# Optimization experiments

Measured on AMD Instinct MI355X. Metric: run time of the kernel, lower is better.

## Reference

```python
import jax, jax.numpy as jnp
import numpy as np
from jax import lax

# ---- module constants (match init_kwargs) ----
B, C, H, W = 8, 32, 128, 128
OUT = 32
RB = 1                      # refer_band
GB = (1, 1)                 # init_guard_band
GB_MAX = 3
PAD = GB[0] + RB            # replication pad on all 4 sides (=2)
KH = GB[0] + GB[1] + 2 * RB # kernel_size[0] = 4
KW = 4                      # kernel_size[1]
N = KH * KW                 # 16 ring sampling points
EPS = 1e-5


def _gen_prf():
    """Ring offsets (top,right,bottom,left blocks), matches _gen_prf_grid."""
    rb, gb = RB, GB
    h_prf = (rb + gb[0]) * 2 + 1
    w_prf = (rb + gb[1]) * 2 + 1
    xs = np.arange(-(rb + gb[0]), rb + gb[0] + 1)
    ys = np.arange(-(rb + gb[1]), rb + gb[1] + 1)
    X, Y = np.meshgrid(xs, ys, indexing='ij')
    def ring(A):
        t = A[0:rb, 0:w_prf - rb]
        r = A[0:h_prf - rb, w_prf - rb:w_prf]
        d = A[h_prf - rb:h_prf, rb:w_prf]
        l = A[rb:h_prf, 0:rb]
        return np.concatenate([t.ravel(), r.ravel(), d.ravel(), l.ravel()])
    return ring(X).astype(np.float32), ring(Y).astype(np.float32)

PRF_X, PRF_Y = _gen_prf()  # each (N,)


def _conv(x, w, b, pad, stride=(1, 1)):
    out = lax.conv_general_dilated(
        x, w, stride, [(pad[0], pad[0]), (pad[1], pad[1])],
        dimension_numbers=('NCHW', 'OIHW', 'NCHW'))
    return out + b[None, :, None, None]


def _bn(x, gamma, beta):
    # training-mode batchnorm (biased variance), matching torch default
    m = jnp.mean(x, (0, 2, 3), keepdims=True)
    v = jnp.var(x, (0, 2, 3), keepdims=True)
    return (x - m) * jax.lax.rsqrt(v + EPS) * gamma[None, :, None, None] + beta[None, :, None, None]


def _sample(x_flat, ix, iy, Wp, h, w):
    # x_flat: (B, C, Hp*Wp); ix, iy: (B, h, w, N) int -> (B, C, h, w, N)
    b = ix.shape[0]
    c = x_flat.shape[1]
    idx = (ix * Wp + iy).reshape(b, 1, -1)
    g = jnp.take_along_axis(x_flat, idx, axis=2)
    return g.reshape(b, c, h, w, N)


def _forward(x, w_vrt, b_vrt, g_vrt, be_vrt, w_hrz, b_hrz, g_hrz, be_hrz, w_pk, b_pk):
    b, c, h, w = x.shape
    x_pad = jnp.pad(x, ((0, 0), (0, 0), (PAD, PAD), (PAD, PAD)), mode='edge')
    Hp, Wp = x_pad.shape[2], x_pad.shape[3]
    x_flat = x_pad.reshape(b, c, Hp * Wp)

    # ---- BandEst: per-pixel guard-band widths in 4 directions (B,4,H,W) ----
    v = jax.nn.sigmoid(_bn(_conv(x, w_vrt, b_vrt, (GB_MAX, 0)), g_vrt, be_vrt)) * (GB_MAX - 1)
    hz = jax.nn.sigmoid(_bn(_conv(x, w_hrz, b_hrz, (0, GB_MAX)), g_hrz, be_hrz)) * (GB_MAX - 1)
    gb = jnp.concatenate([v, hz], axis=1)

    # ---- reference-cell sampling positions p = center + ring + learned move ----
    base_x = (jnp.arange(h, dtype=x.dtype) + PAD)[None, :, None, None]
    base_y = (jnp.arange(w, dtype=x.dtype) + PAD)[None, None, :, None]
    p_x = base_x + jnp.asarray(PRF_X)[None, None, None, :]  # (1,H,1,N)->bcast
    p_y = base_y + jnp.asarray(PRF_Y)[None, None, None, :]

    n4 = N // 4  # points per ring side (t,r,d,l ordering)
    def rep(g2):  # (B,H,W) -> (B,H,W,n4)
        return jnp.broadcast_to(g2[..., None], (b, h, w, n4))
    zeros = jnp.zeros((b, h, w, n4), x.dtype)
    move_x = jnp.concatenate([-rep(gb[:, 0]), zeros, rep(gb[:, 1]), zeros], -1)
    move_y = jnp.concatenate([zeros, rep(gb[:, 3]), zeros, -rep(gb[:, 2])], -1)
    p_x = p_x + move_x  # (B,H,W,N)
    p_y = p_y + move_y

    # ---- bilinear (two-corner) gather, mirrors torch q_lt/q_rb/g_lt/g_rb ----
    q_lt_x = jnp.floor(lax.stop_gradient(p_x))
    q_lt_y = jnp.floor(lax.stop_gradient(p_y))
    q_rb_x, q_rb_y = q_lt_x + 1, q_lt_y + 1
    q_lt_xi = jnp.clip(q_lt_x, 0, Hp - 1).astype(jnp.int32)
    q_lt_yi = jnp.clip(q_lt_y, 0, Wp - 1).astype(jnp.int32)
    q_rb_xi = jnp.clip(q_rb_x, 0, Hp - 1).astype(jnp.int32)
    q_rb_yi = jnp.clip(q_rb_y, 0, Wp - 1).astype(jnp.int32)
    p_x = jnp.clip(p_x, 0, Hp - 1)
    p_y = jnp.clip(p_y, 0, Wp - 1)

    g_lt = (1 + (q_lt_xi.astype(p_x.dtype) - p_x)) * (1 + (q_lt_yi.astype(p_y.dtype) - p_y))
    g_rb = (1 - (q_rb_xi.astype(p_x.dtype) - p_x)) * (1 - (q_rb_yi.astype(p_y.dtype) - p_y))

    x_q_lt = _sample(x_flat, q_lt_xi, q_lt_yi, Wp, h, w)  # (B,C,H,W,N)
    x_q_rb = _sample(x_flat, q_rb_xi, q_rb_yi, Wp, h, w)
    x_r = g_lt[:, None] * x_q_lt + g_rb[:, None] * x_q_rb

    # center value x_c equals x itself (center indices land in the interior)
    x_prf = x[:, :, :, :, None] - x_r  # (B,C,H,W,N)

    # ---- _reshape_x_prf: (B,C,H,W,N) -> (B,C,H*KH,W*KW) ----
    xk = x_prf.reshape(b, c, h, w, KH, KW).transpose(0, 1, 2, 4, 3, 5).reshape(b, c, h * KH, w * KW)

    # ---- peak conv: kernel = stride = (KH,KW), no padding ----
    return _conv(xk, w_pk, b_pk, (0, 0), stride=(KH, KW))


def setup_inputs() -> dict:
    key = jax.random.key(0)
    ks = jax.random.split(key, 8)
    s = 0.05
    return {
        'x': jax.random.normal(ks[0], (B, C, H, W), jnp.float32),
        'w_vrt': jax.random.normal(ks[1], (2, C, 2 * GB_MAX + 1, 1), jnp.float32) * s,
        'b_vrt': jax.random.normal(ks[2], (2,), jnp.float32) * s,
        'g_vrt': jnp.ones((2,), jnp.float32),
        'be_vrt': jnp.zeros((2,), jnp.float32),
        'w_hrz': jax.random.normal(ks[3], (2, C, 1, 2 * GB_MAX + 1), jnp.float32) * s,
        'b_hrz': jax.random.normal(ks[4], (2,), jnp.float32) * s,
        'g_hrz': jnp.ones((2,), jnp.float32),
        'be_hrz': jnp.zeros((2,), jnp.float32),
        'w_pk': jax.random.normal(ks[5], (OUT, C, KH, KW), jnp.float32) * s,
        'b_pk': jax.random.normal(ks[6], (OUT,), jnp.float32) * s,
    }


def reference(x, w_vrt, b_vrt, g_vrt, be_vrt, w_hrz, b_hrz, g_hrz, be_hrz, w_pk, b_pk):
    return _forward(x, w_vrt, b_vrt, g_vrt, be_vrt, w_hrz, b_hrz, g_hrz, be_hrz, w_pk, b_pk)
```

## Files before the change

### kernel.cpp

```cpp
#include <hip/hip_runtime.h>
#include <math.h>

#define BB 8
#define CCH 32
#define HH 128
#define WW 128
#define OUTC 32
#define NPIX (BB*HH*WW)
#define HWP 131
#define NCONVBLK 2048

#define WS_XTB   0
#define WS_CONV4 (BB*HH*WW*CCH/2)
#define WS_PART  (WS_CONV4 + BB*HH*WW*4)
#define WS_WKB   (WS_PART + NCONVBLK*8)

#define TILE_USH (12*40*5*8)

typedef __attribute__((ext_vector_type(8))) short short8;
typedef __attribute__((ext_vector_type(4))) float f32x4;

__device__ __forceinline__ unsigned short f2bf(float f) {
    unsigned u = __float_as_uint(f);
    unsigned r = (u + 0x7FFFu + ((u >> 16) & 1u)) >> 16;
    return (unsigned short)r;
}
__device__ __forceinline__ unsigned cvtpk(float lo, float hi) {
    unsigned r;
    asm("v_cvt_pk_bf16_f32 %0, %1, %2" : "=v"(r) : "v"(lo), "v"(hi));
    return r;
}
__device__ __forceinline__ float bflo(unsigned w) { return __uint_as_float(w << 16); }
__device__ __forceinline__ float bfhi(unsigned w) { return __uint_as_float(w & 0xFFFF0000u); }

__global__ __launch_bounds__(256) void k_fused1(const float* __restrict__ x,
        const float* __restrict__ w_vrt, const float* __restrict__ b_vrt,
        const float* __restrict__ w_hrz, const float* __restrict__ b_hrz,
        const float* __restrict__ w_pk, float* __restrict__ ws) {
    __shared__ float red[4][64][4];
    __shared__ unsigned xrowp[16][65];
    int blk = blockIdx.x, t = threadIdx.x;
    if (blk < NCONVBLK) {
        int cb = blk;
        int idx0 = cb * 64;
        int b = idx0 >> 14, ij0 = idx0 & 16383, i = ij0 >> 7, j0c = ij0 & 127;
        int px = t & 63;
        int grp = __builtin_amdgcn_readfirstlane(t >> 6);
        float v0 = 0.f, v1 = 0.f, h0 = 0.f, h1 = 0.f;
        float cen_prev = 0.f;
        for (int c8 = 0; c8 < 8; c8++) {
            int c = grp * 8 + c8;
            const float* basec = x + ((size_t)(b*CCH + c))*HH*WW;
            #pragma unroll
            for (int k = 0; k < 7; k++) {
                float wv0 = w_vrt[c*7 + k], wv1 = w_vrt[224 + c*7 + k];
                int gr = i + k - 3;
                if (gr >= 0 && gr < HH) {
                    float xv = basec[(size_t)gr*WW + j0c + px];
                    v0 += wv0 * xv; v1 += wv1 * xv;
                    if (k == 3) {
                        if ((c8 & 1) == 0) cen_prev = xv;
                        else xrowp[grp*4 + (c8 >> 1)][px] = cvtpk(cen_prev, xv);
                    }
                }
                float wh0 = w_hrz[c*7 + k], wh1 = w_hrz[224 + c*7 + k];
                int gc = j0c + px + k - 3;
                if (gc >= 0 && gc < WW) {
                    float xh = basec[(size_t)i*WW + gc];
                    h0 += wh0 * xh; h1 += wh1 * xh;
                }
            }
        }
        red[grp][px][0] = v0; red[grp][px][1] = v1;
        red[grp][px][2] = h0; red[grp][px][3] = h1;
        __syncthreads();
        {
            unsigned* xtb4 = (unsigned*)(ws + WS_XTB);
            int bi = b*HH + i;
            #pragma unroll
            for (int u = 0; u < 4; u++) {
                int e = u*256 + t;
                int ppx = e >> 4, cp = e & 15;
                xtb4[((size_t)bi*WW + j0c + ppx)*16 + cp] = xrowp[cp][ppx];
            }
        }
        if (grp == 0) {
            float fv0 = red[0][px][0]+red[1][px][0]+red[2][px][0]+red[3][px][0] + b_vrt[0];
            float fv1 = red[0][px][1]+red[1][px][1]+red[2][px][1]+red[3][px][1] + b_vrt[1];
            float fh0 = red[0][px][2]+red[1][px][2]+red[2][px][2]+red[3][px][2] + b_hrz[0];
            float fh1 = red[0][px][3]+red[1][px][3]+red[2][px][3]+red[3][px][3] + b_hrz[1];
            float4* conv4 = (float4*)(ws + WS_CONV4);
            conv4[idx0 + px] = make_float4(fv0, fv1, fh0, fh1);
            float stv[8] = {fv0, fv1, fh0, fh1, fv0*fv0, fv1*fv1, fh0*fh0, fh1*fh1};
            #pragma unroll
            for (int u = 0; u < 8; u++) {
                float s = stv[u];
                for (int off = 32; off; off >>= 1) s += __shfl_down(s, off);
                if (px == 0) ws[WS_PART + cb*8 + u] = s;
            }
        }
    } else {
        unsigned short* wkb = (unsigned short*)(ws + WS_WKB);
        int e = (blk - NCONVBLK) * 2048 + t;
        for (int u = 0; u < 8; u++, e += 256) {
            int o = e >> 9, n = (e >> 5) & 15, c = e & 31;
            wkb[o*512 + n*32 + c] = f2bf(w_pk[((o*32 + c) << 4) + n]);
        }
    }
}

__device__ __forceinline__ short8 sample_frag(const unsigned short* tile,
        const float* xc8, const float* gbv, float fi, float fj, int n,
        float prx, float pry, int i0, int j0, int quad) {
    float mx = 0.f, my = 0.f;
    if (n < 4)       mx = -gbv[0];
    else if (n < 8)  my =  gbv[3];
    else if (n < 12) mx =  gbv[1];
    else             my = -gbv[2];
    float px = fi + prx + mx;
    float py = fj + pry + my;
    float qlx = floorf(px), qly = floorf(py);
    int qlxi = min(max((int)qlx, 0), HWP);
    int qlyi = min(max((int)qly, 0), HWP);
    int qrxi = min(max((int)qlx + 1, 0), HWP);
    int qryi = min(max((int)qly + 1, 0), HWP);
    float pxc = fminf(fmaxf(px, 0.f), (float)HWP);
    float pyc = fminf(fmaxf(py, 0.f), (float)HWP);
    float glt = (1.f + ((float)qlxi - pxc)) * (1.f + ((float)qlyi - pyc));
    float grb = (1.f - ((float)qrxi - pxc)) * (1.f - ((float)qryi - pyc));
    float nglt = -glt, ngrb = -grb;
    int ltr = min(max(qlxi - 2, 0), HH - 1), ltc = min(max(qlyi - 2, 0), WW - 1);
    int rbr = min(max(qrxi - 2, 0), HH - 1), rbc = min(max(qryi - 2, 0), WW - 1);
    int lt_off = (ltr - i0 + 4)*1600 + (ltc - j0 + 4)*40 + quad*8;
    int rb_off = (rbr - i0 + 4)*1600 + (rbc - j0 + 4)*40 + quad*8;
    uint4 lw = *(const uint4*)(tile + lt_off);
    uint4 rw = *(const uint4*)(tile + rb_off);
    float d0 = fmaf(nglt, bflo(lw.x), fmaf(ngrb, bflo(rw.x), xc8[0]));
    float d1 = fmaf(nglt, bfhi(lw.x), fmaf(ngrb, bfhi(rw.x), xc8[1]));
    float d2 = fmaf(nglt, bflo(lw.y), fmaf(ngrb, bflo(rw.y), xc8[2]));
    float d3 = fmaf(nglt, bfhi(lw.y), fmaf(ngrb, bfhi(rw.y), xc8[3]));
    float d4 = fmaf(nglt, bflo(lw.z), fmaf(ngrb, bflo(rw.z), xc8[4]));
    float d5 = fmaf(nglt, bfhi(lw.z), fmaf(ngrb, bfhi(rw.z), xc8[5]));
    float d6 = fmaf(nglt, bflo(lw.w), fmaf(ngrb, bflo(rw.w), xc8[6]));
    float d7 = fmaf(nglt, bfhi(lw.w), fmaf(ngrb, bfhi(rw.w), xc8[7]));
    uint4 bw;
    bw.x = cvtpk(d0, d1); bw.y = cvtpk(d2, d3);
    bw.z = cvtpk(d4, d5); bw.w = cvtpk(d6, d7);
    return *(short8*)&bw;
}

__device__ __forceinline__ void frac_setup(float pm, float& ng, int& m) {
    float qf = floorf(pm);
    int qi = min(max((int)qf, 0), HWP);
    float pmc = fminf(fmaxf(pm, 0.f), (float)HWP);
    ng = pmc - (float)qi - 1.f;
    m = min(max(qi - 2, 0), HH - 1);
}
__device__ __forceinline__ short8 samp1(const unsigned short* tile,
        const float* xc8, float ng, int off) {
    uint4 lw = *(const uint4*)(tile + off);
    float d0 = fmaf(ng, bflo(lw.x), xc8[0]);
    float d1 = fmaf(ng, bfhi(lw.x), xc8[1]);
    float d2 = fmaf(ng, bflo(lw.y), xc8[2]);
    float d3 = fmaf(ng, bfhi(lw.y), xc8[3]);
    float d4 = fmaf(ng, bflo(lw.z), xc8[4]);
    float d5 = fmaf(ng, bfhi(lw.z), xc8[5]);
    float d6 = fmaf(ng, bflo(lw.w), xc8[6]);
    float d7 = fmaf(ng, bfhi(lw.w), xc8[7]);
    uint4 bw;
    bw.x = cvtpk(d0, d1); bw.y = cvtpk(d2, d3);
    bw.z = cvtpk(d4, d5); bw.w = cvtpk(d6, d7);
    return *(short8*)&bw;
}

__global__ __launch_bounds__(256, 4) void k_main(const float* __restrict__ ws,
        const float* __restrict__ x,
        const float* __restrict__ g_vrt, const float* __restrict__ be_vrt,
        const float* __restrict__ g_hrz, const float* __restrict__ be_hrz,
        const float* __restrict__ b_pk, float* __restrict__ out) {
    __shared__ unsigned short tile[TILE_USH];
    __shared__ float racc[32][8];
    __shared__ float bnab_s[8];
    const unsigned short* xtb = (const unsigned short*)(ws + WS_XTB);
    const unsigned short* wkb = (const unsigned short*)(ws + WS_WKB);
    const float* part = ws + WS_PART;
    const float prfx[16] = {-2,-2,-2,-2, -2,-1, 0, 1,  2, 2, 2, 2, -1, 0, 1, 2};
    const float prfy[16] = {-2,-1, 0, 1,  2, 2, 2, 2, -1, 0, 1, 2, -2,-2,-2,-2};
    const int ioffs[16]  = {-2,-1, 0, 1, -2,-1, 0, 1, -1, 0, 1, 2, -1, 0, 1, 2};

    int t = threadIdx.x;
    int blk = ((blockIdx.x & 7) << 7) | (blockIdx.x >> 3);
    int b = blk >> 7;
    int i0 = ((blk >> 2) & 31) * 4;
    int j0 = (blk & 3) * 32;

    for (int s = t; s < 12*40*4; s += 256) {
        int q = s & 3, cc = (s >> 2) % 40, r = (s >> 2) / 40;
        int gr = min(max(i0 - 4 + r, 0), HH - 1);
        int gc = min(max(j0 - 4 + cc, 0), WW - 1);
        uint4 v = *(const uint4*)(xtb + (((size_t)(b*HH + gr))*WW + gc)*CCH + q*8);
        *(uint4*)(tile + ((r*40 + cc)*5 + q)*8) = v;
    }
    {
        int s8 = t & 7, chunk = t >> 3;
        float sum = 0.f;
        #pragma unroll 8
        for (int m = 0; m < 64; m++)
            sum += part[(size_t)(chunk*64 + m)*8 + s8];
        racc[chunk][s8] = sum;
    }
    __syncthreads();
    if (t < 8) {
        float tot = 0.f;
        #pragma unroll
        for (int c = 0; c < 32; c++) tot += racc[c][t];
        racc[0][t] = tot;
    }
    __syncthreads();
    if (t < 4) {
        const float cnt = (float)NPIX;
        float mean = racc[0][t] / cnt;
        float var  = racc[0][4 + t] / cnt - mean * mean;
        float gamma = (t < 2) ? g_vrt[t] : g_hrz[t - 2];
        float beta  = (t < 2) ? be_vrt[t] : be_hrz[t - 2];
        float a = gamma * rsqrtf(var + 1e-5f);
        bnab_s[t]     = a;
        bnab_s[4 + t] = beta - mean * a;
    }
    __syncthreads();

    int w = t >> 6, pl = t & 15, quad = (t >> 4) & 3;
    int ir = i0 + w;
    int pjA = j0 + pl, pjB = j0 + 16 + pl;
    int pixA = (b << 14) + ir * WW + pjA;
    int pixB = pixA + 16;
    int q8 = quad * 8;

    float xcA[8], xcB[8];
    {
        const float* xb = x + (size_t)b * CCH * HH * WW + (size_t)ir * WW;
        #pragma unroll
        for (int k = 0; k < 8; k++) {
            const float* p = xb + (size_t)(q8 + k) * (HH * WW);
            xcA[k] = p[pjA];
            xcB[k] = p[pjB];
        }
    }
    const float4* conv4 = (const float4*)(ws + WS_CONV4);
    float4 cvA = conv4[pixA], cvB = conv4[pixB];
    float gbvA[4], gbvB[4];
    gbvA[0] = 2.f / (1.f + expf(-(cvA.x * bnab_s[0] + bnab_s[4])));
    gbvA[1] = 2.f / (1.f + expf(-(cvA.y * bnab_s[1] + bnab_s[5])));
    gbvA[2] = 2.f / (1.f + expf(-(cvA.z * bnab_s[2] + bnab_s[6])));
    gbvA[3] = 2.f / (1.f + expf(-(cvA.w * bnab_s[3] + bnab_s[7])));
    gbvB[0] = 2.f / (1.f + expf(-(cvB.x * bnab_s[0] + bnab_s[4])));
    gbvB[1] = 2.f / (1.f + expf(-(cvB.y * bnab_s[1] + bnab_s[5])));
    gbvB[2] = 2.f / (1.f + expf(-(cvB.z * bnab_s[2] + bnab_s[6])));
    gbvB[3] = 2.f / (1.f + expf(-(cvB.w * bnab_s[3] + bnab_s[7])));

    f32x4 accA0 = {0.f,0.f,0.f,0.f}, accA1 = {0.f,0.f,0.f,0.f};
    f32x4 accB0 = {0.f,0.f,0.f,0.f}, accB1 = {0.f,0.f,0.f,0.f};
    float fi = (float)ir + 2.f;
    float fjA = (float)pjA + 2.f, fjB = (float)pjB + 2.f;

    short8 a0 = *(const short8*)(wkb + (size_t)pl * 512 + q8);
    short8 a1 = *(const short8*)(wkb + (size_t)(pl + 16) * 512 + q8);

    float ngA_ = 0.f, ngB_ = 0.f;
    int baseA_ = 0, baseB_ = 0;

    #pragma unroll
    for (int n = 0; n < 16; n++) {
        short8 na0 = a0, na1 = a1;
        if (n < 15) {
            na0 = *(const short8*)(wkb + (size_t)pl * 512 + (n+1)*32 + q8);
            na1 = *(const short8*)(wkb + (size_t)(pl + 16) * 512 + (n+1)*32 + q8);
        }
        if ((n & 3) == 0) {
            int g = n >> 2;
            float pmA, pmB;
            if (g == 0)      { pmA = (fi  - 2.f) - gbvA[0]; pmB = (fi  - 2.f) - gbvB[0]; }
            else if (g == 1) { pmA = (fjA + 2.f) + gbvA[3]; pmB = (fjB + 2.f) + gbvB[3]; }
            else if (g == 2) { pmA = (fi  + 2.f) + gbvA[1]; pmB = (fi  + 2.f) + gbvB[1]; }
            else             { pmA = (fjA - 2.f) - gbvA[2]; pmB = (fjB - 2.f) - gbvB[2]; }
            int mA, mB;
            frac_setup(pmA, ngA_, mA);
            frac_setup(pmB, ngB_, mB);
            if ((g & 1) == 0) {
                baseA_ = (mA - i0 + 4)*1600 + q8;
                baseB_ = (mB - i0 + 4)*1600 + q8;
            } else {
                baseA_ = (mA - j0 + 4)*40 + q8;
                baseB_ = (mB - j0 + 4)*40 + q8;
            }
        }
        short8 bfA, bfB;
        if (n == 11 || n == 15) {
            bfA = sample_frag(tile, xcA, gbvA, fi, fjA, n, prfx[n], prfy[n], i0, j0, quad);
            bfB = sample_frag(tile, xcB, gbvB, fi, fjB, n, prfx[n], prfy[n], i0, j0, quad);
        } else {
            int io = ioffs[n];
            int offA, offB;
            if (((n >> 2) & 1) == 0) {
                int cA = min(max(pjA + io, 0), WW - 1);
                int cB = min(max(pjB + io, 0), WW - 1);
                offA = baseA_ + (cA - j0 + 4)*40;
                offB = baseB_ + (cB - j0 + 4)*40;
            } else {
                int r  = min(max(ir + io, 0), HH - 1);
                int rt = (r - i0 + 4)*1600;
                offA = baseA_ + rt;
                offB = baseB_ + rt;
            }
            bfA = samp1(tile, xcA, ngA_, offA);
            bfB = samp1(tile, xcB, ngB_, offB);
        }
        accA0 = __builtin_amdgcn_mfma_f32_16x16x32_bf16(a0, bfA, accA0, 0, 0, 0);
        accA1 = __builtin_amdgcn_mfma_f32_16x16x32_bf16(a1, bfA, accA1, 0, 0, 0);
        accB0 = __builtin_amdgcn_mfma_f32_16x16x32_bf16(a0, bfB, accB0, 0, 0, 0);
        accB1 = __builtin_amdgcn_mfma_f32_16x16x32_bf16(a1, bfB, accB1, 0, 0, 0);
        a0 = na0; a1 = na1;
    }
    float* opA = out + (size_t)b * (OUTC*HH*WW) + ir * WW + pjA;
    float* opB = opA + 16;
    #pragma unroll
    for (int r = 0; r < 4; r++) {
        int o = quad*4 + r;
        float bo = b_pk[o], bo16 = b_pk[o + 16];
        opA[(size_t)o * (HH*WW)]        = accA0[r] + bo;
        opA[(size_t)(o + 16) * (HH*WW)] = accA1[r] + bo16;
        opB[(size_t)o * (HH*WW)]        = accB0[r] + bo;
        opB[(size_t)(o + 16) * (HH*WW)] = accB1[r] + bo16;
    }
}

extern "C" void kernel_launch(void* const* d_in, const int* in_sizes, int n_in,
                              void* d_out, int out_size, void* d_ws, size_t ws_size,
                              hipStream_t stream) {
    const float* x      = (const float*)d_in[0];
    const float* w_vrt  = (const float*)d_in[1];
    const float* b_vrt  = (const float*)d_in[2];
    const float* g_vrt  = (const float*)d_in[3];
    const float* be_vrt = (const float*)d_in[4];
    const float* w_hrz  = (const float*)d_in[5];
    const float* b_hrz  = (const float*)d_in[6];
    const float* g_hrz  = (const float*)d_in[7];
    const float* be_hrz = (const float*)d_in[8];
    const float* w_pk   = (const float*)d_in[9];
    const float* b_pk   = (const float*)d_in[10];
    float* ws  = (float*)d_ws;
    float* out = (float*)d_out;

    k_fused1<<<NCONVBLK + 8, 256, 0, stream>>>(x, w_vrt, b_vrt, w_hrz, b_hrz, w_pk, ws);
    k_main<<<1024, 256, 0, stream>>>(ws, x, g_vrt, be_vrt, g_hrz, be_hrz, b_pk, out);
}
```

Baseline: 147.1 us.

## Split band-estimation convs into row-strip vertical and row-wise horizontal blocks

Restructures the first kernel into separate block types. Vertical-conv blocks each cover 8 rows and keep 14 input rows in registers, so every loaded value is reused across rows. Horizontal-conv blocks each handle a full row with float2 loads, two pixels per thread. This cuts the redundant 7x global reads per pixel from the old fused per-pixel loop, at the cost of more registers per thread and a changed workspace layout for conv outputs and partial BN statistics.

```diff
diff --git a/kernel.cpp b/kernel.cpp
--- a/kernel.cpp
+++ b/kernel.cpp
@@ -8,12 +8,13 @@
 #define OUTC 32
 #define NPIX (BB*HH*WW)
 #define HWP 131
-#define NCONVBLK 2048
 
 #define WS_XTB   0
-#define WS_CONV4 (BB*HH*WW*CCH/2)
-#define WS_PART  (WS_CONV4 + BB*HH*WW*4)
-#define WS_WKB   (WS_PART + NCONVBLK*8)
+#define WS_VO2   2097152
+#define WS_HO2   (WS_VO2 + NPIX*2)
+#define WS_PARTV (WS_HO2 + NPIX*2)
+#define WS_PARTH (WS_PARTV + 2048*4)
+#define WS_WKB   (WS_PARTH + 1024*4)
 
 #define TILE_USH (12*40*5*8)
 
@@ -37,71 +38,146 @@
         const float* __restrict__ w_vrt, const float* __restrict__ b_vrt,
         const float* __restrict__ w_hrz, const float* __restrict__ b_hrz,
         const float* __restrict__ w_pk, float* __restrict__ ws) {
-    __shared__ float red[4][64][4];
-    __shared__ unsigned xrowp[16][65];
+    __shared__ unsigned sbuf[12288];
     int blk = blockIdx.x, t = threadIdx.x;
-    if (blk < NCONVBLK) {
-        int cb = blk;
-        int idx0 = cb * 64;
-        int b = idx0 >> 14, ij0 = idx0 & 16383, i = ij0 >> 7, j0c = ij0 & 127;
+    if (blk < 256) {
+        int jh = blk & 1, istr = (blk >> 1) & 15, b = blk >> 5;
+        int i0 = istr * 8;
         int px = t & 63;
-        int grp = __builtin_amdgcn_readfirstlane(t >> 6);
-        float v0 = 0.f, v1 = 0.f, h0 = 0.f, h1 = 0.f;
-        float cen_prev = 0.f;
+        int sub = __builtin_amdgcn_readfirstlane(t >> 6);
+        int col = jh * 64 + px;
+        unsigned* xp = sbuf;
+        float* red_v = (float*)(sbuf + 8192);
+        float vo[8][2];
+        #pragma unroll
+        for (int r = 0; r < 8; r++) { vo[r][0] = 0.f; vo[r][1] = 0.f; }
+        float prev[8];
         for (int c8 = 0; c8 < 8; c8++) {
-            int c = grp * 8 + c8;
+            int c = sub * 8 + c8;
             const float* basec = x + ((size_t)(b*CCH + c))*HH*WW;
-            #pragma unroll
-            for (int k = 0; k < 7; k++) {
-                float wv0 = w_vrt[c*7 + k], wv1 = w_vrt[224 + c*7 + k];
-                int gr = i + k - 3;
-                if (gr >= 0 && gr < HH) {
-                    float xv = basec[(size_t)gr*WW + j0c + px];
-                    v0 += wv0 * xv; v1 += wv1 * xv;
-                    if (k == 3) {
-                        if ((c8 & 1) == 0) cen_prev = xv;
-                        else xrowp[grp*4 + (c8 >> 1)][px] = cvtpk(cen_prev, xv);
-                    }
+            float xv[14];
+            #pragma unroll
+            for (int rr = 0; rr < 14; rr++) {
+                int gr = i0 - 3 + rr;
+                xv[rr] = ((unsigned)gr < (unsigned)HH) ? basec[(size_t)gr*WW + col] : 0.f;
+            }
+            #pragma unroll
+            for (int r = 0; r < 8; r++) {
+                #pragma unroll
+                for (int k = 0; k < 7; k++) {
+                    float wv0 = w_vrt[c*7 + k], wv1 = w_vrt[224 + c*7 + k];
+                    vo[r][0] += wv0 * xv[r + k];
+                    vo[r][1] += wv1 * xv[r + k];
                 }
-                float wh0 = w_hrz[c*7 + k], wh1 = w_hrz[224 + c*7 + k];
-                int gc = j0c + px + k - 3;
-                if (gc >= 0 && gc < WW) {
-                    float xh = basec[(size_t)i*WW + gc];
-                    h0 += wh0 * xh; h1 += wh1 * xh;
-                }
-            }
-        }
-        red[grp][px][0] = v0; red[grp][px][1] = v1;
-        red[grp][px][2] = h0; red[grp][px][3] = h1;
+            }
+            if ((c8 & 1) == 0) {
+                #pragma unroll
+                for (int r = 0; r < 8; r++) prev[r] = xv[3 + r];
+            } else {
+                #pragma unroll
+                for (int r = 0; r < 8; r++)
+                    xp[(r*64 + px)*16 + sub*4 + (c8 >> 1)] = cvtpk(prev[r], xv[3 + r]);
+            }
+        }
+        #pragma unroll
+        for (int r = 0; r < 8; r++) {
+            red_v[((sub*64 + px)*8 + r)*2 + 0] = vo[r][0];
+            red_v[((sub*64 + px)*8 + r)*2 + 1] = vo[r][1];
+        }
         __syncthreads();
-        {
-            unsigned* xtb4 = (unsigned*)(ws + WS_XTB);
-            int bi = b*HH + i;
+        float2* vo2 = (float2*)(ws + WS_VO2);
+        #pragma unroll
+        for (int h2 = 0; h2 < 2; h2++) {
+            int r2 = sub * 2 + h2;
+            float fv0 = red_v[((0*64 + px)*8 + r2)*2 + 0] + red_v[((1*64 + px)*8 + r2)*2 + 0]
+                      + red_v[((2*64 + px)*8 + r2)*2 + 0] + red_v[((3*64 + px)*8 + r2)*2 + 0]
+                      + b_vrt[0];
+            float fv1 = red_v[((0*64 + px)*8 + r2)*2 + 1] + red_v[((1*64 + px)*8 + r2)*2 + 1]
+                      + red_v[((2*64 + px)*8 + r2)*2 + 1] + red_v[((3*64 + px)*8 + r2)*2 + 1]
+                      + b_vrt[1];
+            int i = i0 + r2;
+            vo2[(size_t)(b << 14) + i * WW + col] = make_float2(fv0, fv1);
+            int cb = (b*HH + i)*2 + jh;
+            float stv[4] = {fv0, fv1, fv0*fv0, fv1*fv1};
             #pragma unroll
             for (int u = 0; u < 4; u++) {
-                int e = u*256 + t;
-                int ppx = e >> 4, cp = e & 15;
-                xtb4[((size_t)bi*WW + j0c + ppx)*16 + cp] = xrowp[cp][ppx];
-            }
-        }
-        if (grp == 0) {
-            float fv0 = red[0][px][0]+red[1][px][0]+red[2][px][0]+red[3][px][0] + b_vrt[0];
-            float fv1 = red[0][px][1]+red[1][px][1]+red[2][px][1]+red[3][px][1] + b_vrt[1];
-            float fh0 = red[0][px][2]+red[1][px][2]+red[2][px][2]+red[3][px][2] + b_hrz[0];
-            float fh1 = red[0][px][3]+red[1][px][3]+red[2][px][3]+red[3][px][3] + b_hrz[1];
-            float4* conv4 = (float4*)(ws + WS_CONV4);
-            conv4[idx0 + px] = make_float4(fv0, fv1, fh0, fh1);
-            float stv[8] = {fv0, fv1, fh0, fh1, fv0*fv0, fv1*fv1, fh0*fh0, fh1*fh1};
-            #pragma unroll
-            for (int u = 0; u < 8; u++) {
                 float s = stv[u];
                 for (int off = 32; off; off >>= 1) s += __shfl_down(s, off);
-                if (px == 0) ws[WS_PART + cb*8 + u] = s;
+                if (px == 0) ws[WS_PARTV + cb*4 + u] = s;
+            }
+        }
+        {
+            uint4* xtb4 = (uint4*)(ws + WS_XTB);
+            const uint4* xp4 = (const uint4*)xp;
+            #pragma unroll
+            for (int u = 0; u < 8; u++) {
+                int e4 = u*256 + t;
+                int rr = e4 >> 8, rem = e4 & 255, jj = rem >> 2, c4 = rem & 3;
+                xtb4[(size_t)((b*HH + i0 + rr)*WW + jh*64 + jj)*4 + c4]
+                    = xp4[(rr*64 + jj)*4 + c4];
+            }
+        }
+    } else if (blk < 1280) {
+        int e = blk - 256;
+        int b = e >> 7, i = e & 127;
+        int px2 = t & 63;
+        int sub = __builtin_amdgcn_readfirstlane(t >> 6);
+        float* red_h = (float*)sbuf;
+        int cc[5]; bool mv[10];
+        #pragma unroll
+        for (int u = 0; u < 5; u++) {
+            int c2 = 2*px2 - 4 + 2*u;
+            cc[u] = min(max(c2, 0), WW - 2);
+            mv[2*u]   = (unsigned)c2 < (unsigned)WW;
+            mv[2*u+1] = (unsigned)(c2 + 1) < (unsigned)WW;
+        }
+        float h0A = 0.f, h1A = 0.f, h0B = 0.f, h1B = 0.f;
+        for (int c8 = 0; c8 < 8; c8++) {
+            int c = sub * 8 + c8;
+            const float* rowb = x + ((size_t)(b*CCH + c)*HH + i)*WW;
+            float lo[10];
+            #pragma unroll
+            for (int u = 0; u < 5; u++) {
+                float2 v = *(const float2*)(rowb + cc[u]);
+                lo[2*u]   = mv[2*u]   ? v.x : 0.f;
+                lo[2*u+1] = mv[2*u+1] ? v.y : 0.f;
+            }
+            #pragma unroll
+            for (int k = 0; k < 7; k++) {
+                float wh0 = w_hrz[c*7 + k], wh1 = w_hrz[224 + c*7 + k];
+                h0A += wh0 * lo[k+1]; h1A += wh1 * lo[k+1];
+                h0B += wh0 * lo[k+2]; h1B += wh1 * lo[k+2];
+            }
+        }
+        red_h[(sub*64 + px2)*4 + 0] = h0A;
+        red_h[(sub*64 + px2)*4 + 1] = h0B;
+        red_h[(sub*64 + px2)*4 + 2] = h1A;
+        red_h[(sub*64 + px2)*4 + 3] = h1B;
+        __syncthreads();
+        if (sub == 0) {
+            float fh0A = red_h[(0*64+px2)*4+0] + red_h[(1*64+px2)*4+0]
+                       + red_h[(2*64+px2)*4+0] + red_h[(3*64+px2)*4+0] + b_hrz[0];
+            float fh0B = red_h[(0*64+px2)*4+1] + red_h[(1*64+px2)*4+1]
+                       + red_h[(2*64+px2)*4+1] + red_h[(3*64+px2)*4+1] + b_hrz[0];
+            float fh1A = red_h[(0*64+px2)*4+2] + red_h[(1*64+px2)*4+2]
+                       + red_h[(2*64+px2)*4+2] + red_h[(3*64+px2)*4+2] + b_hrz[1];
+            float fh1B = red_h[(0*64+px2)*4+3] + red_h[(1*64+px2)*4+3]
+                       + red_h[(2*64+px2)*4+3] + red_h[(3*64+px2)*4+3] + b_hrz[1];
+            float2* ho2 = (float2*)(ws + WS_HO2);
+            size_t pix = (size_t)(b << 14) + i * WW + 2*px2;
+            *(float4*)(ho2 + pix) = make_float4(fh0A, fh1A, fh0B, fh1B);
+            float stv[4] = {fh0A + fh0B, fh1A + fh1B,
+                            fh0A*fh0A + fh0B*fh0B, fh1A*fh1A + fh1B*fh1B};
+            #pragma unroll
+            for (int u = 0; u < 4; u++) {
+                float s = stv[u];
+                for (int off = 32; off; off >>= 1) s += __shfl_down(s, off);
+                if (px2 == 0) ws[WS_PARTH + e*4 + u] = s;
             }
         }
     } else {
         unsigned short* wkb = (unsigned short*)(ws + WS_WKB);
-        int e = (blk - NCONVBLK) * 2048 + t;
+        int e = (blk - 1280) * 2048 + t;
         for (int u = 0; u < 8; u++, e += 256) {
             int o = e >> 9, n = (e >> 5) & 15, c = e & 31;
             wkb[o*512 + n*32 + c] = f2bf(w_pk[((o*32 + c) << 4) + n]);
@@ -183,7 +259,8 @@
     __shared__ float bnab_s[8];
     const unsigned short* xtb = (const unsigned short*)(ws + WS_XTB);
     const unsigned short* wkb = (const unsigned short*)(ws + WS_WKB);
-    const float* part = ws + WS_PART;
+    const float* partv = ws + WS_PARTV;
+    const float* parth = ws + WS_PARTH;
     const float prfx[16] = {-2,-2,-2,-2, -2,-1, 0, 1,  2, 2, 2, 2, -1, 0, 1, 2};
     const float prfy[16] = {-2,-1, 0, 1,  2, 2, 2, 2, -1, 0, 1, 2, -2,-2,-2,-2};
     const int ioffs[16]  = {-2,-1, 0, 1, -2,-1, 0, 1, -1, 0, 1, 2, -1, 0, 1, 2};
@@ -203,10 +280,16 @@
     }
     {
         int s8 = t & 7, chunk = t >> 3;
+        int col = (s8 & 1) + ((s8 >> 2) << 1);
+        bool isv = ((s8 >> 1) & 1) == 0;
         float sum = 0.f;
-        #pragma unroll 8
-        for (int m = 0; m < 64; m++)
-            sum += part[(size_t)(chunk*64 + m)*8 + s8];
+        if (isv) {
+            for (int m = 0; m < 64; m++)
+                sum += partv[(size_t)(chunk*64 + m)*4 + col];
+        } else {
+            for (int m = 0; m < 32; m++)
+                sum += parth[(size_t)(chunk*32 + m)*4 + col];
+        }
         racc[chunk][s8] = sum;
     }
     __syncthreads();
@@ -246,17 +329,19 @@
             xcB[k] = p[pjB];
         }
     }
-    const float4* conv4 = (const float4*)(ws + WS_CONV4);
-    float4 cvA = conv4[pixA], cvB = conv4[pixB];
+    const float2* vo2 = (const float2*)(ws + WS_VO2);
+    const float2* ho2 = (const float2*)(ws + WS_HO2);
+    float2 vA = vo2[pixA], hA = ho2[pixA];
+    float2 vB = vo2[pixB], hB = ho2[pixB];
     float gbvA[4], gbvB[4];
-    gbvA[0] = 2.f / (1.f + expf(-(cvA.x * bnab_s[0] + bnab_s[4])));
-    gbvA[1] = 2.f / (1.f + expf(-(cvA.y * bnab_s[1] + bnab_s[5])));
-    gbvA[2] = 2.f / (1.f + expf(-(cvA.z * bnab_s[2] + bnab_s[6])));
-    gbvA[3] = 2.f / (1.f + expf(-(cvA.w * bnab_s[3] + bnab_s[7])));
-    gbvB[0] = 2.f / (1.f + expf(-(cvB.x * bnab_s[0] + bnab_s[4])));
-    gbvB[1] = 2.f / (1.f + expf(-(cvB.y * bnab_s[1] + bnab_s[5])));
-    gbvB[2] = 2.f / (1.f + expf(-(cvB.z * bnab_s[2] + bnab_s[6])));
-    gbvB[3] = 2.f / (1.f + expf(-(cvB.w * bnab_s[3] + bnab_s[7])));
+    gbvA[0] = 2.f / (1.f + expf(-(vA.x * bnab_s[0] + bnab_s[4])));
+    gbvA[1] = 2.f / (1.f + expf(-(vA.y * bnab_s[1] + bnab_s[5])));
+    gbvA[2] = 2.f / (1.f + expf(-(hA.x * bnab_s[2] + bnab_s[6])));
+    gbvA[3] = 2.f / (1.f + expf(-(hA.y * bnab_s[3] + bnab_s[7])));
+    gbvB[0] = 2.f / (1.f + expf(-(vB.x * bnab_s[0] + bnab_s[4])));
+    gbvB[1] = 2.f / (1.f + expf(-(vB.y * bnab_s[1] + bnab_s[5])));
+    gbvB[2] = 2.f / (1.f + expf(-(hB.x * bnab_s[2] + bnab_s[6])));
+    gbvB[3] = 2.f / (1.f + expf(-(hB.y * bnab_s[3] + bnab_s[7])));
 
     f32x4 accA0 = {0.f,0.f,0.f,0.f}, accA1 = {0.f,0.f,0.f,0.f};
     f32x4 accB0 = {0.f,0.f,0.f,0.f}, accB1 = {0.f,0.f,0.f,0.f};
@@ -351,6 +436,6 @@
     float* ws  = (float*)d_ws;
     float* out = (float*)d_out;
 
-    k_fused1<<<NCONVBLK + 8, 256, 0, stream>>>(x, w_vrt, b_vrt, w_hrz, b_hrz, w_pk, ws);
+    k_fused1<<<256 + 1024 + 8, 256, 0, stream>>>(x, w_vrt, b_vrt, w_hrz, b_hrz, w_pk, ws);
     k_main<<<1024, 256, 0, stream>>>(ws, x, g_vrt, be_vrt, g_hrz, be_hrz, b_pk, out);
 }
```

New measurement: 128.3 us. -12.8%, faster.
